# Kernel optimization log

Hardware: AMD Instinct MI355X
Metric: run time of the kernel (lower is better)

Reference implementation:

```python
import jax, jax.numpy as jnp
import numpy as np

N, E, T = 10000, 160000, 1600000
D, C, H = 256, 64, 1024  # d_model, d_message/channels, 4*d_model ffn hidden


def setup_inputs() -> dict:
    key = jax.random.key(0)
    ks = jax.random.split(key, 20)
    rn = lambda k, s, sc=1.0: jax.random.normal(k, s, dtype=jnp.float32) * sc
    return {
        "x": rn(ks[0], (N, D)),
        "y": rn(ks[1], (E, D)),
        "r": rn(ks[2], (E, 3)),
        "src": jax.random.randint(ks[3], (E,), 0, N),
        "dst": jax.random.randint(ks[4], (E,), 0, N),
        "tsrc": jax.random.randint(ks[5], (T,), 0, E),
        "tdst": jax.random.randint(ks[6], (T,), 0, E),
        "W_src": rn(ks[7], (D, C), 0.05), "b_src": rn(ks[8], (C,), 0.05),
        "W_dst": rn(ks[9], (D, C), 0.05), "b_dst": rn(ks[10], (C,), 0.05),
        "W_edge": rn(ks[11], (D, C), 0.05), "b_edge": rn(ks[12], (C,), 0.05),
        "attn": rn(ks[13], (C,), 0.05),
        "W1": rn(ks[14], (C, H), 0.05), "b1": rn(ks[15], (H,), 0.05),
        "W2": rn(ks[16], (H, D), 0.05), "b2": rn(ks[17], (D,), 0.05),
    }


def reference(x, y, r, src, dst, tsrc, tdst,
              W_src, b_src, W_dst, b_dst, W_edge, b_edge,
              attn, W1, b1, W2, b2):
    # per-bond message: xij = Lin_src(x)[src] + Lin_dst(x)[dst] + Lin_edge(y)  -> (E, C)
    xij = (x @ W_src + b_src)[src] + (x @ W_dst + b_dst)[dst] + (y @ W_edge + b_edge)

    # triplet angle cosine via normalized (negated) bond vectors  -> (T,)
    rnorm = -r / jnp.linalg.norm(r, axis=1, keepdims=True)
    cos_jik = jnp.clip(jnp.sum(rnorm[tsrc] * rnorm[tdst], axis=-1), -1.0 + 1e-6, 1.0 - 1e-6)

    # Chebyshev expansion: T_n(cos) = cos(n * arccos(cos))  -> (T, C)
    n = jnp.arange(C, dtype=jnp.float32)
    z_jik = jnp.cos(n[None, :] * jnp.arccos(cos_jik)[:, None])

    # triplet feature and attention logit
    e_jik = jax.nn.silu(z_jik + xij[tsrc] + xij[tdst])          # (T, C)
    logits = e_jik @ attn                                        # (T,)

    # segment softmax over triplets grouped by destination bond (edge_softmax)
    mx = jax.ops.segment_max(logits, tdst, num_segments=E)
    ex = jnp.exp(logits - mx[tdst])
    den = jax.ops.segment_sum(ex, tdst, num_segments=E)
    a = ex / den[tdst]                                           # (T,)

    # attention-weighted scatter-sum of neighbor bond features  -> (E, C)
    ft = jax.ops.segment_sum(xij[tsrc] * a[:, None], tdst, num_segments=E)

    # feedforward: Linear -> SiLU -> Linear  -> (E, D)
    return jax.nn.silu(ft @ W1 + b1) @ W2 + b2
```

## Files before the change

kernel.cpp:

```cpp
#include <hip/hip_runtime.h>

#define N_NODES 10000
#define N_EDGES 160000
#define N_TRI   1600000
#define DM      256
#define CH      64
#define HH      1024

typedef short bf16x8 __attribute__((ext_vector_type(8)));
typedef float f32x4  __attribute__((ext_vector_type(4)));

__device__ __forceinline__ unsigned short f2bf(float f) {
  unsigned int u = __float_as_uint(f);
  u += 0x7fff + ((u >> 16) & 1);
  return (unsigned short)(u >> 16);
}

__global__ __launch_bounds__(256) void k_node_proj(
    const float* __restrict__ x, const float* __restrict__ Ws, const float* __restrict__ bs,
    const float* __restrict__ Wd, const float* __restrict__ bd,
    float* __restrict__ xs, float* __restrict__ xd) {
  __shared__ float xl[4][DM];
  int tid = threadIdx.x;
  int n0 = blockIdx.x * 4;
  for (int i = tid; i < 4 * DM; i += 256) xl[i >> 8][i & 255] = x[n0 * DM + i];
  __syncthreads();
  int c = tid & 63, g = tid >> 6;
  float as = bs[c], ad = bd[c];
  for (int d = 0; d < DM; d++) {
    float xv = xl[g][d];
    as += xv * Ws[d * CH + c];
    ad += xv * Wd[d * CH + c];
  }
  int n = n0 + g;
  xs[n * CH + c] = as;
  xd[n * CH + c] = ad;
}

__global__ __launch_bounds__(256) void k_edge_proj(
    const float* __restrict__ y, const float* __restrict__ We, const float* __restrict__ be,
    const float* __restrict__ xs, const float* __restrict__ xd,
    const int* __restrict__ src, const int* __restrict__ dst,
    float* __restrict__ xij) {
  __shared__ float yl[16][DM];
  int tid = threadIdx.x;
  int e0 = blockIdx.x * 16;
  for (int i = tid; i < 16 * DM; i += 256) yl[i >> 8][i & 255] = y[e0 * DM + i];
  __syncthreads();
  int c = tid & 63, g = tid >> 6;
  float acc[4];
#pragma unroll
  for (int s = 0; s < 4; s++) acc[s] = be[c];
  for (int d = 0; d < DM; d += 4) {
    float w0 = We[(d + 0) * CH + c];
    float w1 = We[(d + 1) * CH + c];
    float w2 = We[(d + 2) * CH + c];
    float w3 = We[(d + 3) * CH + c];
#pragma unroll
    for (int s = 0; s < 4; s++) {
      const float4 yv = *(const float4*)&yl[g * 4 + s][d];
      acc[s] += yv.x * w0 + yv.y * w1 + yv.z * w2 + yv.w * w3;
    }
  }
#pragma unroll
  for (int s = 0; s < 4; s++) {
    int e = e0 + g * 4 + s;
    xij[e * CH + c] = acc[s] + xs[src[e] * CH + c] + xd[dst[e] * CH + c];
  }
}

__global__ void k_rnorm(const float* __restrict__ r, float4* __restrict__ rn4) {
  int e = blockIdx.x * 256 + threadIdx.x;
  if (e >= N_EDGES) return;
  float a = r[e * 3 + 0], b = r[e * 3 + 1], c = r[e * 3 + 2];
  float inv = rsqrtf(a * a + b * b + c * c);
  rn4[e] = (float4){-a * inv, -b * inv, -c * inv, 0.f};
}

__global__ __launch_bounds__(256) void k_theta(
    const float4* __restrict__ rn4, const int* __restrict__ tsrc, const int* __restrict__ tdst,
    float* __restrict__ theta) {
  int t = blockIdx.x * 256 + threadIdx.x;
  if (t >= N_TRI) return;
  float4 a = rn4[tsrc[t]];
  float4 b = rn4[tdst[t]];
  float c = a.x * b.x + a.y * b.y + a.z * b.z;
  c = fminf(fmaxf(c, -1.0f + 1e-6f), 1.0f - 1e-6f);
  theta[t] = acosf(c);
}

__global__ void k_hist(const int* __restrict__ tdst, int* __restrict__ cnt) {
  int t = blockIdx.x * 256 + threadIdx.x;
  if (t < N_TRI) atomicAdd(&cnt[tdst[t]], 1);
}

__global__ __launch_bounds__(256) void k_scan_sum(const int* __restrict__ cnt,
                                                  int* __restrict__ bsum, int n) {
  __shared__ int s[256];
  int b = blockIdx.x, tid = threadIdx.x;
  int tot = 0;
#pragma unroll
  for (int i = 0; i < 8; i++) {
    int idx = b * 2048 + i * 256 + tid;
    if (idx < n) tot += cnt[idx];
  }
  s[tid] = tot;
  __syncthreads();
  for (int off = 128; off > 0; off >>= 1) {
    if (tid < off) s[tid] += s[tid + off];
    __syncthreads();
  }
  if (tid == 0) bsum[b] = s[0];
}

__global__ void k_scan_top(int* __restrict__ bsum, int nb, int* __restrict__ start_last) {
  if (threadIdx.x == 0) {
    int run = 0;
    for (int i = 0; i < nb; i++) {
      int v = bsum[i];
      bsum[i] = run;
      run += v;
    }
    *start_last = run;
  }
}

__global__ __launch_bounds__(256) void k_scan_apply(const int* __restrict__ cnt,
                                                    const int* __restrict__ bsum,
                                                    int* __restrict__ start,
                                                    int* __restrict__ cur, int n) {
  __shared__ int s[256];
  int b = blockIdx.x, tid = threadIdx.x;
  int base = b * 2048 + tid * 8;
  int loc[8];
  int tot = 0;
#pragma unroll
  for (int i = 0; i < 8; i++) {
    int idx = base + i;
    int v = (idx < n) ? cnt[idx] : 0;
    loc[i] = tot;
    tot += v;
  }
  s[tid] = tot;
  __syncthreads();
  for (int off = 1; off < 256; off <<= 1) {
    int t2 = 0;
    if (tid >= off) t2 = s[tid - off];
    __syncthreads();
    if (tid >= off) s[tid] += t2;
    __syncthreads();
  }
  int excl = s[tid] - tot + bsum[b];
#pragma unroll
  for (int i = 0; i < 8; i++) {
    int idx = base + i;
    if (idx < n) {
      int v = excl + loc[i];
      start[idx] = v;
      cur[idx] = v;
    }
  }
}

__global__ void k_scatter(const int* __restrict__ tdst, int* __restrict__ cur,
                          int* __restrict__ sorted) {
  int t = blockIdx.x * 256 + threadIdx.x;
  if (t < N_TRI) {
    int p = atomicAdd(&cur[tdst[t]], 1);
    sorted[p] = t;
  }
}

__global__ __launch_bounds__(256) void k_logits(
    const float* __restrict__ theta, const int* __restrict__ tsrc, const int* __restrict__ tdst,
    const float* __restrict__ xij, const float* __restrict__ attn,
    float* __restrict__ logits) {
  int tid = threadIdx.x;
  int t = blockIdx.x * 4 + (tid >> 6);
  int lane = tid & 63;
  float th = theta[t];
  int ts = tsrc[t], td = tdst[t];
  float z = __cosf(th * (float)lane);
  float v = z + xij[ts * CH + lane] + xij[td * CH + lane];
  float sv = v / (1.0f + __expf(-v));
  float contrib = sv * attn[lane];
#pragma unroll
  for (int off = 32; off; off >>= 1) contrib += __shfl_xor(contrib, off);
  if (lane == 0) logits[t] = contrib;
}

__global__ __launch_bounds__(256) void k_softmax_ft(
    const int* __restrict__ start, const int* __restrict__ sorted,
    const float* __restrict__ logits, const int* __restrict__ tsrc,
    const float* __restrict__ xij, unsigned short* __restrict__ ft) {
  int tid = threadIdx.x;
  int e = blockIdx.x * 4 + (tid >> 6);
  int lane = tid & 63;
  int beg = start[e], end = start[e + 1];
  int deg = end - beg;
  float acc = 0.f;
  if (deg > 0) {
    if (deg <= 64) {
      int t = 0;
      float l = -1e30f;
      int ts_ = 0;
      if (lane < deg) {
        t = sorted[beg + lane];
        l = logits[t];
        ts_ = tsrc[t];
      }
      float mx = l;
#pragma unroll
      for (int off = 32; off; off >>= 1) mx = fmaxf(mx, __shfl_xor(mx, off));
      float ex = (lane < deg) ? __expf(l - mx) : 0.f;
      float den = ex;
#pragma unroll
      for (int off = 32; off; off >>= 1) den += __shfl_xor(den, off);
      float p = ex / den;
      for (int i = 0; i < deg; i++) {
        int tsi = __shfl(ts_, i);
        float ai = __shfl(p, i);
        acc += ai * xij[tsi * CH + lane];
      }
    } else {
      float mx = -1e30f;
      for (int i = lane; i < deg; i += 64) mx = fmaxf(mx, logits[sorted[beg + i]]);
#pragma unroll
      for (int off = 32; off; off >>= 1) mx = fmaxf(mx, __shfl_xor(mx, off));
      float den = 0.f;
      for (int i = lane; i < deg; i += 64) den += __expf(logits[sorted[beg + i]] - mx);
#pragma unroll
      for (int off = 32; off; off >>= 1) den += __shfl_xor(den, off);
      for (int i = 0; i < deg; i++) {
        int tt = sorted[beg + i];
        float ai = __expf(logits[tt] - mx) / den;
        acc += ai * xij[tsrc[tt] * CH + lane];
      }
    }
  }
  ft[e * CH + lane] = f2bf(acc);
}

__global__ __launch_bounds__(256) void k_prep_w1t(const float* __restrict__ W1,
                                                  unsigned short* __restrict__ W1T) {
  int idx = blockIdx.x * 256 + threadIdx.x;
  int n = idx >> 6, k = idx & 63;
  W1T[idx] = f2bf(W1[k * HH + n]);
}

__global__ __launch_bounds__(256) void k_prep_w2t(const float* __restrict__ W2,
                                                  unsigned short* __restrict__ W2T) {
  int idx = blockIdx.x * 256 + threadIdx.x;
  int n = idx >> 10, k = idx & 1023;
  W2T[idx] = f2bf(W2[k * DM + n]);
}

#define HL_STRIDE 72
__global__ __launch_bounds__(256) void k_ffn_mfma(
    const unsigned short* __restrict__ ft, const unsigned short* __restrict__ W1T,
    const float* __restrict__ b1, const unsigned short* __restrict__ W2T,
    const float* __restrict__ b2, float* __restrict__ out) {
  __shared__ unsigned short ftl[64 * 64];
  __shared__ unsigned short hl[2][64 * HL_STRIDE];
  int tid = threadIdx.x;
  int wave = tid >> 6, lane = tid & 63;
  int l16 = lane & 15, lq = lane >> 4;
  int e0 = blockIdx.x * 64;

  {
    const uint* g = (const uint*)(ft + (size_t)e0 * CH);
    uint* s = (uint*)ftl;
    for (int i = tid; i < 64 * 32; i += 256) s[i] = g[i];
  }
  __syncthreads();

  bf16x8 aft[4][2];
#pragma unroll
  for (int mt = 0; mt < 4; mt++)
#pragma unroll
    for (int s = 0; s < 2; s++)
      aft[mt][s] = *(const bf16x8*)&ftl[(mt * 16 + l16) * 64 + s * 32 + lq * 8];

  f32x4 acc[4][4];
#pragma unroll
  for (int mt = 0; mt < 4; mt++)
#pragma unroll
    for (int nt = 0; nt < 4; nt++) acc[mt][nt] = (f32x4){0.f, 0.f, 0.f, 0.f};

  for (int cc = 0; cc < 16; cc++) {
    int p = cc & 1;
    {
      int ncol = cc * 64 + wave * 16 + l16;
      const unsigned short* wp = &W1T[ncol * 64 + lq * 8];
      bf16x8 bw0 = *(const bf16x8*)wp;
      bf16x8 bw1 = *(const bf16x8*)(wp + 32);
      float b1v = b1[ncol];
#pragma unroll
      for (int mt = 0; mt < 4; mt++) {
        f32x4 h = (f32x4){0.f, 0.f, 0.f, 0.f};
        h = __builtin_amdgcn_mfma_f32_16x16x32_bf16(aft[mt][0], bw0, h, 0, 0, 0);
        h = __builtin_amdgcn_mfma_f32_16x16x32_bf16(aft[mt][1], bw1, h, 0, 0, 0);
#pragma unroll
        for (int r = 0; r < 4; r++) {
          float v = h[r] + b1v;
          float sv = v / (1.f + __expf(-v));
          hl[p][(mt * 16 + lq * 4 + r) * HL_STRIDE + wave * 16 + l16] = f2bf(sv);
        }
      }
    }
    __syncthreads();
#pragma unroll
    for (int nt = 0; nt < 4; nt++) {
      const unsigned short* wp =
          &W2T[(size_t)(wave * 64 + nt * 16 + l16) * HH + cc * 64 + lq * 8];
      bf16x8 b0 = *(const bf16x8*)wp;
      bf16x8 b1f = *(const bf16x8*)(wp + 32);
#pragma unroll
      for (int mt = 0; mt < 4; mt++) {
        bf16x8 a0 = *(const bf16x8*)&hl[p][(mt * 16 + l16) * HL_STRIDE + lq * 8];
        bf16x8 a1 = *(const bf16x8*)&hl[p][(mt * 16 + l16) * HL_STRIDE + 32 + lq * 8];
        acc[mt][nt] = __builtin_amdgcn_mfma_f32_16x16x32_bf16(a0, b0, acc[mt][nt], 0, 0, 0);
        acc[mt][nt] = __builtin_amdgcn_mfma_f32_16x16x32_bf16(a1, b1f, acc[mt][nt], 0, 0, 0);
      }
    }
  }

#pragma unroll
  for (int nt = 0; nt < 4; nt++) {
    int col = wave * 64 + nt * 16 + l16;
    float b2v = b2[col];
#pragma unroll
    for (int mt = 0; mt < 4; mt++) {
      int row = e0 + mt * 16 + lq * 4;
#pragma unroll
      for (int r = 0; r < 4; r++)
        out[(size_t)(row + r) * DM + col] = acc[mt][nt][r] + b2v;
    }
  }
}

extern "C" void kernel_launch(void* const* d_in, const int* in_sizes, int n_in,
                              void* d_out, int out_size, void* d_ws, size_t ws_size,
                              hipStream_t stream) {
  (void)in_sizes; (void)n_in; (void)out_size; (void)ws_size;
  const float* x      = (const float*)d_in[0];
  const float* y      = (const float*)d_in[1];
  const float* r      = (const float*)d_in[2];
  const int*   src    = (const int*)d_in[3];
  const int*   dst    = (const int*)d_in[4];
  const int*   tsrc   = (const int*)d_in[5];
  const int*   tdst   = (const int*)d_in[6];
  const float* W_src  = (const float*)d_in[7];
  const float* b_src  = (const float*)d_in[8];
  const float* W_dst  = (const float*)d_in[9];
  const float* b_dst  = (const float*)d_in[10];
  const float* W_edge = (const float*)d_in[11];
  const float* b_edge = (const float*)d_in[12];
  const float* attn   = (const float*)d_in[13];
  const float* W1     = (const float*)d_in[14];
  const float* b1     = (const float*)d_in[15];
  const float* W2     = (const float*)d_in[16];
  const float* b2     = (const float*)d_in[17];
  float* out = (float*)d_out;

  char* wsp = (char*)d_ws;
  auto alloc = [&](size_t bytes) -> char* {
    char* p = wsp;
    wsp += (bytes + 255) & ~(size_t)255;
    return p;
  };
  float* xs     = (float*)alloc((size_t)N_NODES * CH * 4);
  float* xd     = (float*)alloc((size_t)N_NODES * CH * 4);
  float* xij    = (float*)alloc((size_t)N_EDGES * CH * 4);
  float4* rn4   = (float4*)alloc((size_t)N_EDGES * 16);
  float* theta  = (float*)alloc((size_t)N_TRI * 4);
  float* logits = (float*)alloc((size_t)N_TRI * 4);
  int*   cnt    = (int*)alloc((size_t)N_EDGES * 4);
  int*   start  = (int*)alloc((size_t)(N_EDGES + 1) * 4);
  int*   cur    = (int*)alloc((size_t)N_EDGES * 4);
  int*   bsum   = (int*)alloc(1024 * 4);
  int*   sorted = (int*)alloc((size_t)N_TRI * 4);
  unsigned short* ftb = (unsigned short*)alloc((size_t)N_EDGES * CH * 2);
  unsigned short* W1T = (unsigned short*)alloc((size_t)CH * HH * 2);
  unsigned short* W2T = (unsigned short*)alloc((size_t)HH * DM * 2);

  const int NB = (N_EDGES + 2047) / 2048;

  k_prep_w1t<<<(CH * HH) / 256, 256, 0, stream>>>(W1, W1T);
  k_prep_w2t<<<(HH * DM) / 256, 256, 0, stream>>>(W2, W2T);

  k_node_proj<<<N_NODES / 4, 256, 0, stream>>>(x, W_src, b_src, W_dst, b_dst, xs, xd);
  k_rnorm<<<N_EDGES / 256, 256, 0, stream>>>(r, rn4);
  k_edge_proj<<<N_EDGES / 16, 256, 0, stream>>>(y, W_edge, b_edge, xs, xd, src, dst, xij);
  k_theta<<<N_TRI / 256, 256, 0, stream>>>(rn4, tsrc, tdst, theta);

  hipMemsetAsync(cnt, 0, (size_t)N_EDGES * 4, stream);
  k_hist<<<N_TRI / 256, 256, 0, stream>>>(tdst, cnt);
  k_scan_sum<<<NB, 256, 0, stream>>>(cnt, bsum, N_EDGES);
  k_scan_top<<<1, 64, 0, stream>>>(bsum, NB, &start[N_EDGES]);
  k_scan_apply<<<NB, 256, 0, stream>>>(cnt, bsum, start, cur, N_EDGES);
  k_scatter<<<N_TRI / 256, 256, 0, stream>>>(tdst, cur, sorted);

  k_logits<<<N_TRI / 4, 256, 0, stream>>>(theta, tsrc, tdst, xij, attn, logits);
  k_softmax_ft<<<N_EDGES / 4, 256, 0, stream>>>(start, sorted, logits, tsrc, xij, ftb);
  k_ffn_mfma<<<N_EDGES / 64, 256, 0, stream>>>(ftb, W1T, b1, W2T, b2, out);
}
```

Measured before the change: 1.395 ms.

## Fuse logits and segment softmax into one online-softmax kernel per bond

Merges the per-triplet logit kernel into the per-destination-bond softmax/aggregation kernel using an online (running max) softmax. Each wave loads its destination bond's xij once and reuses it across all incoming triplets, prefetching the next source row while computing the current one. This drops the logits buffer and its write/read round trip, and removes a separate launch with 1.6M waves. Separately, the FFN kernel hoists the LDS A-fragment loads out of the nt loop so they are read once instead of four times. The cost is a serial per-triplet dependency chain with a wave reduction and two exps per step, which may limit latency hiding.

```diff
diff --git a/kernel.cpp b/kernel.cpp
--- a/kernel.cpp
+++ b/kernel.cpp
@@ -171,74 +171,72 @@
   }
 }
 
-__global__ __launch_bounds__(256) void k_logits(
-    const float* __restrict__ theta, const int* __restrict__ tsrc, const int* __restrict__ tdst,
+__global__ __launch_bounds__(256) void k_attn_ft(
+    const int* __restrict__ start, const int* __restrict__ sorted,
+    const float* __restrict__ theta, const int* __restrict__ tsrc,
     const float* __restrict__ xij, const float* __restrict__ attn,
-    float* __restrict__ logits) {
-  int tid = threadIdx.x;
-  int t = blockIdx.x * 4 + (tid >> 6);
-  int lane = tid & 63;
-  float th = theta[t];
-  int ts = tsrc[t], td = tdst[t];
-  float z = __cosf(th * (float)lane);
-  float v = z + xij[ts * CH + lane] + xij[td * CH + lane];
-  float sv = v / (1.0f + __expf(-v));
-  float contrib = sv * attn[lane];
-#pragma unroll
-  for (int off = 32; off; off >>= 1) contrib += __shfl_xor(contrib, off);
-  if (lane == 0) logits[t] = contrib;
-}
-
-__global__ __launch_bounds__(256) void k_softmax_ft(
-    const int* __restrict__ start, const int* __restrict__ sorted,
-    const float* __restrict__ logits, const int* __restrict__ tsrc,
-    const float* __restrict__ xij, unsigned short* __restrict__ ft) {
+    unsigned short* __restrict__ ft) {
   int tid = threadIdx.x;
   int e = blockIdx.x * 4 + (tid >> 6);
   int lane = tid & 63;
+  float lanef = (float)lane;
   int beg = start[e], end = start[e + 1];
   int deg = end - beg;
-  float acc = 0.f;
-  if (deg > 0) {
-    if (deg <= 64) {
-      int t = 0;
-      float l = -1e30f;
-      int ts_ = 0;
-      if (lane < deg) {
-        t = sorted[beg + lane];
-        l = logits[t];
-        ts_ = tsrc[t];
+  float xd = xij[e * CH + lane];
+  float av = attn[lane];
+  float m = -1e30f, den = 0.f, acc = 0.f;
+  if (deg > 0 && deg <= 64) {
+    int ts_ = 0;
+    float th_ = 0.f;
+    if (lane < deg) {
+      int t = sorted[beg + lane];
+      ts_ = tsrc[t];
+      th_ = theta[t];
+    }
+    int ts_cur = __shfl(ts_, 0);
+    float th_cur = __shfl(th_, 0);
+    float xs_cur = xij[ts_cur * CH + lane];
+    for (int i = 0; i < deg; i++) {
+      float th_nxt = 0.f, xs_nxt = 0.f;
+      if (i + 1 < deg) {
+        int ts_nxt = __shfl(ts_, i + 1);
+        th_nxt = __shfl(th_, i + 1);
+        xs_nxt = xij[ts_nxt * CH + lane];
       }
-      float mx = l;
-#pragma unroll
-      for (int off = 32; off; off >>= 1) mx = fmaxf(mx, __shfl_xor(mx, off));
-      float ex = (lane < deg) ? __expf(l - mx) : 0.f;
-      float den = ex;
-#pragma unroll
-      for (int off = 32; off; off >>= 1) den += __shfl_xor(den, off);
-      float p = ex / den;
-      for (int i = 0; i < deg; i++) {
-        int tsi = __shfl(ts_, i);
-        float ai = __shfl(p, i);
-        acc += ai * xij[tsi * CH + lane];
-      }
-    } else {
-      float mx = -1e30f;
-      for (int i = lane; i < deg; i += 64) mx = fmaxf(mx, logits[sorted[beg + i]]);
-#pragma unroll
-      for (int off = 32; off; off >>= 1) mx = fmaxf(mx, __shfl_xor(mx, off));
-      float den = 0.f;
-      for (int i = lane; i < deg; i += 64) den += __expf(logits[sorted[beg + i]] - mx);
-#pragma unroll
-      for (int off = 32; off; off >>= 1) den += __shfl_xor(den, off);
-      for (int i = 0; i < deg; i++) {
-        int tt = sorted[beg + i];
-        float ai = __expf(logits[tt] - mx) / den;
-        acc += ai * xij[tsrc[tt] * CH + lane];
-      }
-    }
-  }
-  ft[e * CH + lane] = f2bf(acc);
+      float v = __cosf(th_cur * lanef) + xs_cur + xd;
+      float sv = v / (1.f + __expf(-v));
+      float contrib = sv * av;
+#pragma unroll
+      for (int off = 32; off; off >>= 1) contrib += __shfl_xor(contrib, off);
+      float mn = fmaxf(m, contrib);
+      float scale = __expf(m - mn);
+      float p = __expf(contrib - mn);
+      den = den * scale + p;
+      acc = acc * scale + p * xs_cur;
+      m = mn;
+      th_cur = th_nxt;
+      xs_cur = xs_nxt;
+    }
+  } else if (deg > 64) {
+    for (int i = 0; i < deg; i++) {
+      int t = sorted[beg + i];
+      int ts = tsrc[t];
+      float th = theta[t];
+      float xs = xij[ts * CH + lane];
+      float v = __cosf(th * lanef) + xs + xd;
+      float sv = v / (1.f + __expf(-v));
+      float contrib = sv * av;
+#pragma unroll
+      for (int off = 32; off; off >>= 1) contrib += __shfl_xor(contrib, off);
+      float mn = fmaxf(m, contrib);
+      float scale = __expf(m - mn);
+      float p = __expf(contrib - mn);
+      den = den * scale + p;
+      acc = acc * scale + p * xs;
+      m = mn;
+    }
+  }
+  ft[e * CH + lane] = f2bf(deg > 0 ? acc / den : 0.f);
 }
 
 __global__ __launch_bounds__(256) void k_prep_w1t(const float* __restrict__ W1,
@@ -309,6 +307,12 @@
       }
     }
     __syncthreads();
+    bf16x8 ha[4][2];
+#pragma unroll
+    for (int mt = 0; mt < 4; mt++) {
+      ha[mt][0] = *(const bf16x8*)&hl[p][(mt * 16 + l16) * HL_STRIDE + lq * 8];
+      ha[mt][1] = *(const bf16x8*)&hl[p][(mt * 16 + l16) * HL_STRIDE + 32 + lq * 8];
+    }
 #pragma unroll
     for (int nt = 0; nt < 4; nt++) {
       const unsigned short* wp =
@@ -317,10 +321,8 @@
       bf16x8 b1f = *(const bf16x8*)(wp + 32);
 #pragma unroll
       for (int mt = 0; mt < 4; mt++) {
-        bf16x8 a0 = *(const bf16x8*)&hl[p][(mt * 16 + l16) * HL_STRIDE + lq * 8];
-        bf16x8 a1 = *(const bf16x8*)&hl[p][(mt * 16 + l16) * HL_STRIDE + 32 + lq * 8];
-        acc[mt][nt] = __builtin_amdgcn_mfma_f32_16x16x32_bf16(a0, b0, acc[mt][nt], 0, 0, 0);
-        acc[mt][nt] = __builtin_amdgcn_mfma_f32_16x16x32_bf16(a1, b1f, acc[mt][nt], 0, 0, 0);
+        acc[mt][nt] = __builtin_amdgcn_mfma_f32_16x16x32_bf16(ha[mt][0], b0, acc[mt][nt], 0, 0, 0);
+        acc[mt][nt] = __builtin_amdgcn_mfma_f32_16x16x32_bf16(ha[mt][1], b1f, acc[mt][nt], 0, 0, 0);
       }
     }
   }
@@ -374,7 +376,6 @@
   float* xij    = (float*)alloc((size_t)N_EDGES * CH * 4);
   float4* rn4   = (float4*)alloc((size_t)N_EDGES * 16);
   float* theta  = (float*)alloc((size_t)N_TRI * 4);
-  float* logits = (float*)alloc((size_t)N_TRI * 4);
   int*   cnt    = (int*)alloc((size_t)N_EDGES * 4);
   int*   start  = (int*)alloc((size_t)(N_EDGES + 1) * 4);
   int*   cur    = (int*)alloc((size_t)N_EDGES * 4);
@@ -401,7 +402,6 @@
   k_scan_apply<<<NB, 256, 0, stream>>>(cnt, bsum, start, cur, N_EDGES);
   k_scatter<<<N_TRI / 256, 256, 0, stream>>>(tdst, cur, sorted);
 
-  k_logits<<<N_TRI / 4, 256, 0, stream>>>(theta, tsrc, tdst, xij, attn, logits);
-  k_softmax_ft<<<N_EDGES / 4, 256, 0, stream>>>(start, sorted, logits, tsrc, xij, ftb);
+  k_attn_ft<<<N_EDGES / 4, 256, 0, stream>>>(start, sorted, theta, tsrc, xij, attn, ftb);
   k_ffn_mfma<<<N_EDGES / 64, 256, 0, stream>>>(ftb, W1T, b1, W2T, b2, out);
 }
```

Measured after the change: 1.189 ms. 1.17x faster.
